# Optimization experiments

Measured on AMD Instinct MI355X. Metric: run time of the kernel, lower is better.

## Reference

```python
import jax, jax.numpy as jnp
import numpy as np

N_NODES = 50000
N_EDGES = 625000
D = 128
H = 128

def setup_inputs() -> dict:
    key = jax.random.key(0)
    ks = jax.random.split(key, 6)
    z = jax.random.normal(ks[0], (N_NODES, D), dtype=jnp.float32)
    edge_index = jax.random.randint(ks[1], (2, N_EDGES), 0, N_NODES, dtype=jnp.int64)
    # MLP params (Linear stores y = x @ W + b here; W is [in, out])
    W1 = jax.random.normal(ks[2], (2 * D, H), dtype=jnp.float32) * (1.0 / np.sqrt(2 * D))
    b1 = jnp.zeros((H,), dtype=jnp.float32)
    W2 = jax.random.normal(ks[3], (H, H // 2), dtype=jnp.float32) * (1.0 / np.sqrt(H))
    b2 = jnp.zeros((H // 2,), dtype=jnp.float32)
    W3 = jax.random.normal(ks[4], (H // 2, 1), dtype=jnp.float32) * (1.0 / np.sqrt(H // 2))
    b3 = jnp.zeros((1,), dtype=jnp.float32)
    return {"z": z, "edge_index": edge_index, "W1": W1, "b1": b1,
            "W2": W2, "b2": b2, "W3": W3, "b3": b3}

def reference(z, edge_index, W1, b1, W2, b2, W3, b3):
    # Gather edge endpoints: z_i [E, D], z_j [E, D]
    z_i = z[edge_index[0]]
    z_j = z[edge_index[1]]
    edge_feat = jnp.concatenate([z_i, z_j], axis=-1)  # [E, 2D]
    h = jax.nn.relu(edge_feat @ W1 + b1)              # [E, H]  (dropout = identity, eval)
    h = jax.nn.relu(h @ W2 + b2)                      # [E, H//2]
    scores = (h @ W3 + b3)[:, 0]                      # [E]
    return scores
```

## Files before the change

### kernel.cpp

```cpp
#include <hip/hip_runtime.h>

#define NEDGE 625000
#define NNODE 50000
#define NTILES ((NEDGE + 127) / 128)
#define WPITCH 136
#define EPITCH 68

typedef __bf16 bf16x8 __attribute__((ext_vector_type(8)));
typedef __bf16 bf16x4 __attribute__((ext_vector_type(4)));
typedef unsigned short u16x8 __attribute__((ext_vector_type(8)));
typedef float f32x4 __attribute__((ext_vector_type(4)));
typedef float f32x8 __attribute__((ext_vector_type(8)));

__device__ __forceinline__ unsigned short f32_bf16(float f) {
  unsigned int u = __float_as_uint(f);
  u += 0x7FFFu + ((u >> 16) & 1u);
  return (unsigned short)(u >> 16);
}

__device__ __forceinline__ bf16x8 addrelu8(u16x8 ua, u16x8 ub) {
  bf16x8 a = *(bf16x8*)&ua, b = *(bf16x8*)&ub;
  bf16x8 s = a + b;
  const bf16x8 z = {(__bf16)0.f, (__bf16)0.f, (__bf16)0.f, (__bf16)0.f,
                    (__bf16)0.f, (__bf16)0.f, (__bf16)0.f, (__bf16)0.f};
  return __builtin_elementwise_max(s, z);
}

__global__ __launch_bounds__(256) void prep_kernel(
    const float* __restrict__ W1, const float* __restrict__ W2,
    const int* __restrict__ ei,
    unsigned short* __restrict__ WcatT, unsigned short* __restrict__ W2T,
    int* __restrict__ idx64_flag)
{
  int i = blockIdx.x * 256 + threadIdx.x;
  if (i < 256 * 128) {
    int jp = i >> 7, k = i & 127;
    float v = (jp < 128) ? W1[k * 128 + jp] : W1[(128 + k) * 128 + (jp - 128)];
    WcatT[jp * 128 + k] = f32_bf16(v);
  } else if (i < 256 * 128 + 64 * 128) {
    int i2 = i - 256 * 128;
    int n = i2 >> 7, k = i2 & 127;
    W2T[n * 128 + k] = f32_bf16(W2[k * 64 + n]);
  }
  if (i == 0) {
    int allz = 1;
    for (int j = 1; j < 64; j += 2) allz &= (ei[j] == 0);
    *idx64_flag = allz;
  }
}

__global__ __launch_bounds__(256) void uv_kernel(
    const float* __restrict__ z, const float* __restrict__ b1,
    const unsigned short* __restrict__ WcatT,
    unsigned short* __restrict__ UV)
{
  __shared__ unsigned short st[4 * 32 * EPITCH];
  const int t = threadIdx.x, wave = t >> 6, lane = t & 63, c = lane & 15, q = lane >> 4;
  const int nc = wave;
  const int mbase = blockIdx.x * 32;
  const int rA = mbase + c, rB = mbase + 16 + c;
  const int rAc = (rA < NNODE) ? rA : 0;
  const int rBc = (rB < NNODE) ? rB : 0;

  bf16x8 a0[4], a1[4];
  {
    const float* zA = z + (size_t)rAc * 128 + q * 8;
    const float* zB = z + (size_t)rBc * 128 + q * 8;
#pragma unroll
    for (int kt = 0; kt < 4; ++kt) {
      f32x8 vA = *(const f32x8*)(zA + kt * 32);
      f32x8 vB = *(const f32x8*)(zB + kt * 32);
      a0[kt] = __builtin_convertvector(vA, bf16x8);
      a1[kt] = __builtin_convertvector(vB, bf16x8);
    }
  }

  f32x4 acc[2][4];
#pragma unroll
  for (int mt = 0; mt < 2; ++mt)
#pragma unroll
    for (int nt = 0; nt < 4; ++nt) {
      f32x4 zz = {0.f, 0.f, 0.f, 0.f};
      acc[mt][nt] = zz;
    }

#pragma unroll
  for (int kt = 0; kt < 4; ++kt) {
#pragma unroll
    for (int nt = 0; nt < 4; ++nt) {
      bf16x8 bb = *(const bf16x8*)(WcatT + (size_t)(nc * 64 + nt * 16 + c) * 128 + kt * 32 + q * 8);
      acc[0][nt] = __builtin_amdgcn_mfma_f32_16x16x32_bf16(a0[kt], bb, acc[0][nt], 0, 0, 0);
      acc[1][nt] = __builtin_amdgcn_mfma_f32_16x16x32_bf16(a1[kt], bb, acc[1][nt], 0, 0, 0);
    }
  }

  float badd[4];
#pragma unroll
  for (int nt = 0; nt < 4; ++nt) {
    int col = nc * 64 + nt * 16 + c;
    badd[nt] = (col < 128) ? b1[col] : 0.f;
  }

  unsigned short* my = &st[wave * 32 * EPITCH];
#pragma unroll
  for (int mt = 0; mt < 2; ++mt)
#pragma unroll
    for (int nt = 0; nt < 4; ++nt) {
      f32x4 v = acc[mt][nt];
      f32x4 vb = {v[0] + badd[nt], v[1] + badd[nt], v[2] + badd[nt], v[3] + badd[nt]};
      bf16x4 bv = __builtin_convertvector(vb, bf16x4);
      const unsigned short* pv = (const unsigned short*)&bv;
#pragma unroll
      for (int reg = 0; reg < 4; ++reg)
        my[(mt * 16 + q * 4 + reg) * EPITCH + nt * 16 + c] = pv[reg];
    }
  __asm__ volatile("s_waitcnt lgkmcnt(0)" ::: "memory");

  {
    int lrow = lane >> 1, half = lane & 1;
    int grow = mbase + lrow;
    u16x8 d0 = *(u16x8*)&my[lrow * EPITCH + half * 32 + 0];
    u16x8 d1 = *(u16x8*)&my[lrow * EPITCH + half * 32 + 8];
    u16x8 d2 = *(u16x8*)&my[lrow * EPITCH + half * 32 + 16];
    u16x8 d3 = *(u16x8*)&my[lrow * EPITCH + half * 32 + 24];
    if (grow < NNODE) {
      u16x8* dst = (u16x8*)(UV + (size_t)grow * 256 + nc * 64 + half * 32);
      dst[0] = d0; dst[1] = d1; dst[2] = d2; dst[3] = d3;
    }
  }
}

__global__ __launch_bounds__(256) void edge_kernel(
    const int* __restrict__ ei,
    const unsigned short* __restrict__ UV,
    const unsigned short* __restrict__ W2T,
    const float* __restrict__ b2, const float* __restrict__ W3,
    const float* __restrict__ b3, const int* __restrict__ idx64_flag,
    float* __restrict__ out)
{
  __shared__ unsigned short lW[64 * WPITCH];
  const int t = threadIdx.x, wave = t >> 6, lane = t & 63, c = lane & 15, q = lane >> 4;

  {
    int n = t >> 2, qd = t & 3;
    const u16x8* src = (const u16x8*)(W2T + n * 128 + qd * 32);
    u16x8* dst = (u16x8*)(&lW[n * WPITCH + qd * 32]);
#pragma unroll
    for (int i = 0; i < 4; ++i) dst[i] = src[i];
  }
  __syncthreads();

  const int ebase = blockIdx.x * 128 + wave * 32;
  const int eA = ebase + c, eB = ebase + 16 + c;
  const int eAc = (eA < NEDGE) ? eA : 0;
  const int eBc = (eB < NEDGE) ? eB : 0;
  int sA, dA, sB, dB;
  if (*idx64_flag) {
    const long long* e64 = (const long long*)ei;
    sA = (int)e64[eAc]; dA = (int)e64[NEDGE + eAc];
    sB = (int)e64[eBc]; dB = (int)e64[NEDGE + eBc];
  } else {
    sA = ei[eAc]; dA = ei[NEDGE + eAc];
    sB = ei[eBc]; dB = ei[NEDGE + eBc];
  }

  const u16x8* pAu = (const u16x8*)(UV + (size_t)sA * 256) + q;
  const u16x8* pAv = (const u16x8*)(UV + (size_t)dA * 256 + 128) + q;
  const u16x8* pBu = (const u16x8*)(UV + (size_t)sB * 256) + q;
  const u16x8* pBv = (const u16x8*)(UV + (size_t)dB * 256 + 128) + q;
  u16x8 rAu[4], rAv[4], rBu[4], rBv[4];
#pragma unroll
  for (int kt = 0; kt < 4; ++kt) {
    rAu[kt] = pAu[kt * 4];
    rAv[kt] = pAv[kt * 4];
    rBu[kt] = pBu[kt * 4];
    rBv[kt] = pBv[kt * 4];
  }

  f32x4 acc[2][4];
#pragma unroll
  for (int mt = 0; mt < 2; ++mt)
#pragma unroll
    for (int nt = 0; nt < 4; ++nt) {
      f32x4 zz = {0.f, 0.f, 0.f, 0.f};
      acc[mt][nt] = zz;
    }

#pragma unroll
  for (int kt = 0; kt < 4; ++kt) {
    bf16x8 a0 = addrelu8(rAu[kt], rAv[kt]);
    bf16x8 a1 = addrelu8(rBu[kt], rBv[kt]);
#pragma unroll
    for (int nt = 0; nt < 4; ++nt) {
      bf16x8 bb = *(const bf16x8*)(&lW[(nt * 16 + c) * WPITCH + kt * 32 + q * 8]);
      acc[0][nt] = __builtin_amdgcn_mfma_f32_16x16x32_bf16(a0, bb, acc[0][nt], 0, 0, 0);
      acc[1][nt] = __builtin_amdgcn_mfma_f32_16x16x32_bf16(a1, bb, acc[1][nt], 0, 0, 0);
    }
  }

  float b2v[4], w3v[4];
#pragma unroll
  for (int nt = 0; nt < 4; ++nt) {
    int n = nt * 16 + c;
    b2v[nt] = b2[n];
    w3v[nt] = W3[n];
  }
  const float bias3 = b3[0];

#pragma unroll
  for (int mt = 0; mt < 2; ++mt) {
    float p0 = 0.f, p1 = 0.f, p2 = 0.f, p3 = 0.f;
#pragma unroll
    for (int nt = 0; nt < 4; ++nt) {
      p0 += fmaxf(acc[mt][nt][0] + b2v[nt], 0.f) * w3v[nt];
      p1 += fmaxf(acc[mt][nt][1] + b2v[nt], 0.f) * w3v[nt];
      p2 += fmaxf(acc[mt][nt][2] + b2v[nt], 0.f) * w3v[nt];
      p3 += fmaxf(acc[mt][nt][3] + b2v[nt], 0.f) * w3v[nt];
    }
#pragma unroll
    for (int m = 1; m < 16; m <<= 1) {
      p0 += __shfl_xor(p0, m, 64);
      p1 += __shfl_xor(p1, m, 64);
      p2 += __shfl_xor(p2, m, 64);
      p3 += __shfl_xor(p3, m, 64);
    }
    if (c == 0) {
      int eb = ebase + mt * 16 + q * 4;
      if (eb + 0 < NEDGE) out[eb + 0] = p0 + bias3;
      if (eb + 1 < NEDGE) out[eb + 1] = p1 + bias3;
      if (eb + 2 < NEDGE) out[eb + 2] = p2 + bias3;
      if (eb + 3 < NEDGE) out[eb + 3] = p3 + bias3;
    }
  }
}

extern "C" void kernel_launch(void* const* d_in, const int* in_sizes, int n_in,
                              void* d_out, int out_size, void* d_ws, size_t ws_size,
                              hipStream_t stream) {
  const float* z  = (const float*)d_in[0];
  const int*   ei = (const int*)d_in[1];
  const float* W1 = (const float*)d_in[2];
  const float* b1 = (const float*)d_in[3];
  const float* W2 = (const float*)d_in[4];
  const float* b2 = (const float*)d_in[5];
  const float* W3 = (const float*)d_in[6];
  const float* b3 = (const float*)d_in[7];
  float* out = (float*)d_out;

  unsigned short* UV    = (unsigned short*)d_ws;
  unsigned short* WcatT = UV + (size_t)NNODE * 256;
  unsigned short* W2T   = WcatT + 256 * 128;
  int* idx64_flag       = (int*)(W2T + 64 * 128);

  prep_kernel<<<dim3(160), dim3(256), 0, stream>>>(W1, W2, ei, WcatT, W2T, idx64_flag);
  uv_kernel<<<dim3((NNODE + 31) / 32), dim3(256), 0, stream>>>(z, b1, WcatT, UV);
  edge_kernel<<<dim3(NTILES), dim3(256), 0, stream>>>(
      ei, UV, W2T, b2, W3, b3, idx64_flag, out);
}
```

Measured before the change: 160.2 us.

## Fuse prep, node-projection and edge kernels into one cooperative persistent kernel

Merges the three launches into a single cooperative kernel that uses grid-wide syncs between the weight conversion, the per-node UV projection and the edge MLP phases. Blocks become persistent and loop over node and edge tiles, and the W2 tile is loaded into LDS once per block instead of once per edge tile. The aim is to remove launch gaps and repeated LDS weight staging. The cost is two grid barriers, a grid capped by occupancy queries, and an occupancy query on the host at every launch.

```diff
diff --git a/kernel.cpp b/kernel.cpp
--- a/kernel.cpp
+++ b/kernel.cpp
@@ -1,8 +1,12 @@
 #include <hip/hip_runtime.h>
+#include <hip/hip_cooperative_groups.h>
+
+namespace cg = cooperative_groups;
 
 #define NEDGE 625000
 #define NNODE 50000
 #define NTILES ((NEDGE + 127) / 128)
+#define NMTILES ((NNODE + 31) / 32)
 #define WPITCH 136
 #define EPITCH 68
 
@@ -26,176 +30,122 @@
   return __builtin_elementwise_max(s, z);
 }
 
-__global__ __launch_bounds__(256) void prep_kernel(
-    const float* __restrict__ W1, const float* __restrict__ W2,
-    const int* __restrict__ ei,
-    unsigned short* __restrict__ WcatT, unsigned short* __restrict__ W2T,
-    int* __restrict__ idx64_flag)
+__global__ __launch_bounds__(256, 4) void fused_kernel(
+    const float* __restrict__ z, const int* __restrict__ ei,
+    const float* __restrict__ W1, const float* __restrict__ b1,
+    const float* __restrict__ W2, const float* __restrict__ b2,
+    const float* __restrict__ W3, const float* __restrict__ b3,
+    unsigned short* __restrict__ UV, unsigned short* __restrict__ WcatT,
+    unsigned short* __restrict__ W2T, float* __restrict__ out)
 {
-  int i = blockIdx.x * 256 + threadIdx.x;
-  if (i < 256 * 128) {
-    int jp = i >> 7, k = i & 127;
-    float v = (jp < 128) ? W1[k * 128 + jp] : W1[(128 + k) * 128 + (jp - 128)];
-    WcatT[jp * 128 + k] = f32_bf16(v);
-  } else if (i < 256 * 128 + 64 * 128) {
-    int i2 = i - 256 * 128;
-    int n = i2 >> 7, k = i2 & 127;
-    W2T[n * 128 + k] = f32_bf16(W2[k * 64 + n]);
-  }
-  if (i == 0) {
-    int allz = 1;
-    for (int j = 1; j < 64; j += 2) allz &= (ei[j] == 0);
-    *idx64_flag = allz;
-  }
-}
-
-__global__ __launch_bounds__(256) void uv_kernel(
-    const float* __restrict__ z, const float* __restrict__ b1,
-    const unsigned short* __restrict__ WcatT,
-    unsigned short* __restrict__ UV)
-{
-  __shared__ unsigned short st[4 * 32 * EPITCH];
+  __shared__ unsigned short smem[8704];
+  cg::grid_group grid = cg::this_grid();
   const int t = threadIdx.x, wave = t >> 6, lane = t & 63, c = lane & 15, q = lane >> 4;
-  const int nc = wave;
-  const int mbase = blockIdx.x * 32;
-  const int rA = mbase + c, rB = mbase + 16 + c;
-  const int rAc = (rA < NNODE) ? rA : 0;
-  const int rBc = (rB < NNODE) ? rB : 0;
-
-  bf16x8 a0[4], a1[4];
-  {
-    const float* zA = z + (size_t)rAc * 128 + q * 8;
-    const float* zB = z + (size_t)rBc * 128 + q * 8;
+
+  for (int i = blockIdx.x * 256 + t; i < 256 * 128 + 64 * 128; i += gridDim.x * 256) {
+    if (i < 256 * 128) {
+      int jp = i >> 7, k = i & 127;
+      float v = (jp < 128) ? W1[k * 128 + jp] : W1[(128 + k) * 128 + (jp - 128)];
+      WcatT[jp * 128 + k] = f32_bf16(v);
+    } else {
+      int i2 = i - 256 * 128;
+      int n = i2 >> 7, k = i2 & 127;
+      W2T[n * 128 + k] = f32_bf16(W2[k * 64 + n]);
+    }
+  }
+  grid.sync();
+
+  for (int mtile = blockIdx.x; mtile < NMTILES; mtile += gridDim.x) {
+    const int nc = wave;
+    const int mbase = mtile * 32;
+    const int rA = mbase + c, rB = mbase + 16 + c;
+    const int rAc = (rA < NNODE) ? rA : 0;
+    const int rBc = (rB < NNODE) ? rB : 0;
+
+    bf16x8 a0[4], a1[4];
+    {
+      const float* zA = z + (size_t)rAc * 128 + q * 8;
+      const float* zB = z + (size_t)rBc * 128 + q * 8;
+#pragma unroll
+      for (int kt = 0; kt < 4; ++kt) {
+        f32x8 vA = *(const f32x8*)(zA + kt * 32);
+        f32x8 vB = *(const f32x8*)(zB + kt * 32);
+        a0[kt] = __builtin_convertvector(vA, bf16x8);
+        a1[kt] = __builtin_convertvector(vB, bf16x8);
+      }
+    }
+
+    f32x4 acc[2][4];
+#pragma unroll
+    for (int mt = 0; mt < 2; ++mt)
+#pragma unroll
+      for (int nt = 0; nt < 4; ++nt) {
+        f32x4 zz = {0.f, 0.f, 0.f, 0.f};
+        acc[mt][nt] = zz;
+      }
+
 #pragma unroll
     for (int kt = 0; kt < 4; ++kt) {
-      f32x8 vA = *(const f32x8*)(zA + kt * 32);
-      f32x8 vB = *(const f32x8*)(zB + kt * 32);
-      a0[kt] = __builtin_convertvector(vA, bf16x8);
-      a1[kt] = __builtin_convertvector(vB, bf16x8);
-    }
-  }
-
-  f32x4 acc[2][4];
-#pragma unroll
-  for (int mt = 0; mt < 2; ++mt)
+#pragma unroll
+      for (int nt = 0; nt < 4; ++nt) {
+        bf16x8 bb = *(const bf16x8*)(WcatT + (size_t)(nc * 64 + nt * 16 + c) * 128 + kt * 32 + q * 8);
+        acc[0][nt] = __builtin_amdgcn_mfma_f32_16x16x32_bf16(a0[kt], bb, acc[0][nt], 0, 0, 0);
+        acc[1][nt] = __builtin_amdgcn_mfma_f32_16x16x32_bf16(a1[kt], bb, acc[1][nt], 0, 0, 0);
+      }
+    }
+
+    float badd[4];
 #pragma unroll
     for (int nt = 0; nt < 4; ++nt) {
-      f32x4 zz = {0.f, 0.f, 0.f, 0.f};
-      acc[mt][nt] = zz;
-    }
-
-#pragma unroll
-  for (int kt = 0; kt < 4; ++kt) {
-#pragma unroll
-    for (int nt = 0; nt < 4; ++nt) {
-      bf16x8 bb = *(const bf16x8*)(WcatT + (size_t)(nc * 64 + nt * 16 + c) * 128 + kt * 32 + q * 8);
-      acc[0][nt] = __builtin_amdgcn_mfma_f32_16x16x32_bf16(a0[kt], bb, acc[0][nt], 0, 0, 0);
-      acc[1][nt] = __builtin_amdgcn_mfma_f32_16x16x32_bf16(a1[kt], bb, acc[1][nt], 0, 0, 0);
-    }
-  }
-
-  float badd[4];
-#pragma unroll
-  for (int nt = 0; nt < 4; ++nt) {
-    int col = nc * 64 + nt * 16 + c;
-    badd[nt] = (col < 128) ? b1[col] : 0.f;
-  }
-
-  unsigned short* my = &st[wave * 32 * EPITCH];
-#pragma unroll
-  for (int mt = 0; mt < 2; ++mt)
-#pragma unroll
-    for (int nt = 0; nt < 4; ++nt) {
-      f32x4 v = acc[mt][nt];
-      f32x4 vb = {v[0] + badd[nt], v[1] + badd[nt], v[2] + badd[nt], v[3] + badd[nt]};
-      bf16x4 bv = __builtin_convertvector(vb, bf16x4);
-      const unsigned short* pv = (const unsigned short*)&bv;
-#pragma unroll
-      for (int reg = 0; reg < 4; ++reg)
-        my[(mt * 16 + q * 4 + reg) * EPITCH + nt * 16 + c] = pv[reg];
-    }
-  __asm__ volatile("s_waitcnt lgkmcnt(0)" ::: "memory");
-
-  {
-    int lrow = lane >> 1, half = lane & 1;
-    int grow = mbase + lrow;
-    u16x8 d0 = *(u16x8*)&my[lrow * EPITCH + half * 32 + 0];
-    u16x8 d1 = *(u16x8*)&my[lrow * EPITCH + half * 32 + 8];
-    u16x8 d2 = *(u16x8*)&my[lrow * EPITCH + half * 32 + 16];
-    u16x8 d3 = *(u16x8*)&my[lrow * EPITCH + half * 32 + 24];
-    if (grow < NNODE) {
-      u16x8* dst = (u16x8*)(UV + (size_t)grow * 256 + nc * 64 + half * 32);
-      dst[0] = d0; dst[1] = d1; dst[2] = d2; dst[3] = d3;
-    }
-  }
-}
-
-__global__ __launch_bounds__(256) void edge_kernel(
-    const int* __restrict__ ei,
-    const unsigned short* __restrict__ UV,
-    const unsigned short* __restrict__ W2T,
-    const float* __restrict__ b2, const float* __restrict__ W3,
-    const float* __restrict__ b3, const int* __restrict__ idx64_flag,
-    float* __restrict__ out)
-{
-  __shared__ unsigned short lW[64 * WPITCH];
-  const int t = threadIdx.x, wave = t >> 6, lane = t & 63, c = lane & 15, q = lane >> 4;
+      int col = nc * 64 + nt * 16 + c;
+      badd[nt] = (col < 128) ? b1[col] : 0.f;
+    }
+
+    unsigned short* my = &smem[wave * 32 * EPITCH];
+#pragma unroll
+    for (int mt = 0; mt < 2; ++mt)
+#pragma unroll
+      for (int nt = 0; nt < 4; ++nt) {
+        f32x4 v = acc[mt][nt];
+        f32x4 vb = {v[0] + badd[nt], v[1] + badd[nt], v[2] + badd[nt], v[3] + badd[nt]};
+        bf16x4 bv = __builtin_convertvector(vb, bf16x4);
+        const unsigned short* pv = (const unsigned short*)&bv;
+#pragma unroll
+        for (int reg = 0; reg < 4; ++reg)
+          my[(mt * 16 + q * 4 + reg) * EPITCH + nt * 16 + c] = pv[reg];
+      }
+    __asm__ volatile("s_waitcnt lgkmcnt(0)" ::: "memory");
+
+    {
+      int lrow = lane >> 1, half = lane & 1;
+      int grow = mbase + lrow;
+      u16x8 d0 = *(u16x8*)&my[lrow * EPITCH + half * 32 + 0];
+      u16x8 d1 = *(u16x8*)&my[lrow * EPITCH + half * 32 + 8];
+      u16x8 d2 = *(u16x8*)&my[lrow * EPITCH + half * 32 + 16];
+      u16x8 d3 = *(u16x8*)&my[lrow * EPITCH + half * 32 + 24];
+      if (grow < NNODE) {
+        u16x8* dst = (u16x8*)(UV + (size_t)grow * 256 + nc * 64 + half * 32);
+        dst[0] = d0; dst[1] = d1; dst[2] = d2; dst[3] = d3;
+      }
+    }
+    __asm__ volatile("s_waitcnt lgkmcnt(0)" ::: "memory");
+  }
+  grid.sync();
 
   {
     int n = t >> 2, qd = t & 3;
     const u16x8* src = (const u16x8*)(W2T + n * 128 + qd * 32);
-    u16x8* dst = (u16x8*)(&lW[n * WPITCH + qd * 32]);
+    u16x8* dst = (u16x8*)(&smem[n * WPITCH + qd * 32]);
 #pragma unroll
     for (int i = 0; i < 4; ++i) dst[i] = src[i];
   }
   __syncthreads();
 
-  const int ebase = blockIdx.x * 128 + wave * 32;
-  const int eA = ebase + c, eB = ebase + 16 + c;
-  const int eAc = (eA < NEDGE) ? eA : 0;
-  const int eBc = (eB < NEDGE) ? eB : 0;
-  int sA, dA, sB, dB;
-  if (*idx64_flag) {
-    const long long* e64 = (const long long*)ei;
-    sA = (int)e64[eAc]; dA = (int)e64[NEDGE + eAc];
-    sB = (int)e64[eBc]; dB = (int)e64[NEDGE + eBc];
-  } else {
-    sA = ei[eAc]; dA = ei[NEDGE + eAc];
-    sB = ei[eBc]; dB = ei[NEDGE + eBc];
-  }
-
-  const u16x8* pAu = (const u16x8*)(UV + (size_t)sA * 256) + q;
-  const u16x8* pAv = (const u16x8*)(UV + (size_t)dA * 256 + 128) + q;
-  const u16x8* pBu = (const u16x8*)(UV + (size_t)sB * 256) + q;
-  const u16x8* pBv = (const u16x8*)(UV + (size_t)dB * 256 + 128) + q;
-  u16x8 rAu[4], rAv[4], rBu[4], rBv[4];
-#pragma unroll
-  for (int kt = 0; kt < 4; ++kt) {
-    rAu[kt] = pAu[kt * 4];
-    rAv[kt] = pAv[kt * 4];
-    rBu[kt] = pBu[kt * 4];
-    rBv[kt] = pBv[kt * 4];
-  }
-
-  f32x4 acc[2][4];
-#pragma unroll
-  for (int mt = 0; mt < 2; ++mt)
-#pragma unroll
-    for (int nt = 0; nt < 4; ++nt) {
-      f32x4 zz = {0.f, 0.f, 0.f, 0.f};
-      acc[mt][nt] = zz;
-    }
-
-#pragma unroll
-  for (int kt = 0; kt < 4; ++kt) {
-    bf16x8 a0 = addrelu8(rAu[kt], rAv[kt]);
-    bf16x8 a1 = addrelu8(rBu[kt], rBv[kt]);
-#pragma unroll
-    for (int nt = 0; nt < 4; ++nt) {
-      bf16x8 bb = *(const bf16x8*)(&lW[(nt * 16 + c) * WPITCH + kt * 32 + q * 8]);
-      acc[0][nt] = __builtin_amdgcn_mfma_f32_16x16x32_bf16(a0, bb, acc[0][nt], 0, 0, 0);
-      acc[1][nt] = __builtin_amdgcn_mfma_f32_16x16x32_bf16(a1, bb, acc[1][nt], 0, 0, 0);
-    }
+  int is64;
+  {
+    int allz = 1;
+    for (int j = 1; j < 64; j += 2) allz &= (ei[j] == 0);
+    is64 = allz;
   }
 
   float b2v[4], w3v[4];
@@ -207,29 +157,79 @@
   }
   const float bias3 = b3[0];
 
-#pragma unroll
-  for (int mt = 0; mt < 2; ++mt) {
-    float p0 = 0.f, p1 = 0.f, p2 = 0.f, p3 = 0.f;
-#pragma unroll
-    for (int nt = 0; nt < 4; ++nt) {
-      p0 += fmaxf(acc[mt][nt][0] + b2v[nt], 0.f) * w3v[nt];
-      p1 += fmaxf(acc[mt][nt][1] + b2v[nt], 0.f) * w3v[nt];
-      p2 += fmaxf(acc[mt][nt][2] + b2v[nt], 0.f) * w3v[nt];
-      p3 += fmaxf(acc[mt][nt][3] + b2v[nt], 0.f) * w3v[nt];
-    }
-#pragma unroll
-    for (int m = 1; m < 16; m <<= 1) {
-      p0 += __shfl_xor(p0, m, 64);
-      p1 += __shfl_xor(p1, m, 64);
-      p2 += __shfl_xor(p2, m, 64);
-      p3 += __shfl_xor(p3, m, 64);
-    }
-    if (c == 0) {
-      int eb = ebase + mt * 16 + q * 4;
-      if (eb + 0 < NEDGE) out[eb + 0] = p0 + bias3;
-      if (eb + 1 < NEDGE) out[eb + 1] = p1 + bias3;
-      if (eb + 2 < NEDGE) out[eb + 2] = p2 + bias3;
-      if (eb + 3 < NEDGE) out[eb + 3] = p3 + bias3;
+  for (int tile = blockIdx.x; tile < NTILES; tile += gridDim.x) {
+    const int ebase = tile * 128 + wave * 32;
+    const int eA = ebase + c, eB = ebase + 16 + c;
+    const int eAc = (eA < NEDGE) ? eA : 0;
+    const int eBc = (eB < NEDGE) ? eB : 0;
+    int sA, dA, sB, dB;
+    if (is64) {
+      const long long* e64 = (const long long*)ei;
+      sA = (int)e64[eAc]; dA = (int)e64[NEDGE + eAc];
+      sB = (int)e64[eBc]; dB = (int)e64[NEDGE + eBc];
+    } else {
+      sA = ei[eAc]; dA = ei[NEDGE + eAc];
+      sB = ei[eBc]; dB = ei[NEDGE + eBc];
+    }
+
+    const u16x8* pAu = (const u16x8*)(UV + (size_t)sA * 256) + q;
+    const u16x8* pAv = (const u16x8*)(UV + (size_t)dA * 256 + 128) + q;
+    const u16x8* pBu = (const u16x8*)(UV + (size_t)sB * 256) + q;
+    const u16x8* pBv = (const u16x8*)(UV + (size_t)dB * 256 + 128) + q;
+    u16x8 rAu[4], rAv[4], rBu[4], rBv[4];
+#pragma unroll
+    for (int kt = 0; kt < 4; ++kt) {
+      rAu[kt] = pAu[kt * 4];
+      rAv[kt] = pAv[kt * 4];
+      rBu[kt] = pBu[kt * 4];
+      rBv[kt] = pBv[kt * 4];
+    }
+
+    f32x4 acc[2][4];
+#pragma unroll
+    for (int mt = 0; mt < 2; ++mt)
+#pragma unroll
+      for (int nt = 0; nt < 4; ++nt) {
+        f32x4 zz = {0.f, 0.f, 0.f, 0.f};
+        acc[mt][nt] = zz;
+      }
+
+#pragma unroll
+    for (int kt = 0; kt < 4; ++kt) {
+      bf16x8 a0 = addrelu8(rAu[kt], rAv[kt]);
+      bf16x8 a1 = addrelu8(rBu[kt], rBv[kt]);
+#pragma unroll
+      for (int nt = 0; nt < 4; ++nt) {
+        bf16x8 bb = *(const bf16x8*)(&smem[(nt * 16 + c) * WPITCH + kt * 32 + q * 8]);
+        acc[0][nt] = __builtin_amdgcn_mfma_f32_16x16x32_bf16(a0, bb, acc[0][nt], 0, 0, 0);
+        acc[1][nt] = __builtin_amdgcn_mfma_f32_16x16x32_bf16(a1, bb, acc[1][nt], 0, 0, 0);
+      }
+    }
+
+#pragma unroll
+    for (int mt = 0; mt < 2; ++mt) {
+      float p0 = 0.f, p1 = 0.f, p2 = 0.f, p3 = 0.f;
+#pragma unroll
+      for (int nt = 0; nt < 4; ++nt) {
+        p0 += fmaxf(acc[mt][nt][0] + b2v[nt], 0.f) * w3v[nt];
+        p1 += fmaxf(acc[mt][nt][1] + b2v[nt], 0.f) * w3v[nt];
+        p2 += fmaxf(acc[mt][nt][2] + b2v[nt], 0.f) * w3v[nt];
+        p3 += fmaxf(acc[mt][nt][3] + b2v[nt], 0.f) * w3v[nt];
+      }
+#pragma unroll
+      for (int m = 1; m < 16; m <<= 1) {
+        p0 += __shfl_xor(p0, m, 64);
+        p1 += __shfl_xor(p1, m, 64);
+        p2 += __shfl_xor(p2, m, 64);
+        p3 += __shfl_xor(p3, m, 64);
+      }
+      if (c == 0) {
+        int eb = ebase + mt * 16 + q * 4;
+        if (eb + 0 < NEDGE) out[eb + 0] = p0 + bias3;
+        if (eb + 1 < NEDGE) out[eb + 1] = p1 + bias3;
+        if (eb + 2 < NEDGE) out[eb + 2] = p2 + bias3;
+        if (eb + 3 < NEDGE) out[eb + 3] = p3 + bias3;
+      }
     }
   }
 }
@@ -250,10 +250,16 @@
   unsigned short* UV    = (unsigned short*)d_ws;
   unsigned short* WcatT = UV + (size_t)NNODE * 256;
   unsigned short* W2T   = WcatT + 256 * 128;
-  int* idx64_flag       = (int*)(W2T + 64 * 128);
-
-  prep_kernel<<<dim3(160), dim3(256), 0, stream>>>(W1, W2, ei, WcatT, W2T, idx64_flag);
-  uv_kernel<<<dim3((NNODE + 31) / 32), dim3(256), 0, stream>>>(z, b1, WcatT, UV);
-  edge_kernel<<<dim3(NTILES), dim3(256), 0, stream>>>(
-      ei, UV, W2T, b2, W3, b3, idx64_flag, out);
-}
+
+  int maxB = 0;
+  hipOccupancyMaxActiveBlocksPerMultiprocessor(&maxB, (const void*)fused_kernel, 256, 0);
+  if (maxB < 1) maxB = 1;
+  if (maxB > 4) maxB = 4;
+  int grid = maxB * 256;
+
+  void* args[] = {(void*)&z, (void*)&ei, (void*)&W1, (void*)&b1,
+                  (void*)&W2, (void*)&b2, (void*)&W3, (void*)&b3,
+                  (void*)&UV, (void*)&WcatT, (void*)&W2T, (void*)&out};
+  hipLaunchCooperativeKernel((const void*)fused_kernel, dim3(grid), dim3(256),
+                             args, 0, stream);
+}
```

Measured after the change: 320.6 us. 100% more time.

## Persistent grid for edge kernel and coalesced LDS staging of z in uv kernel

Applied to the files above, without the earlier changes.

The edge kernel now runs a fixed grid of 2048 blocks that loop over edge tiles. Each block loads W2 into shared memory once and reuses it across tiles, instead of reloading it in every one of ~4900 blocks. Launch bounds now request 8 blocks per CU. The uv kernel stages z rows into LDS as bf16 with coalesced loads before MFMA. The cost is a barrier, and the serial tile loop may expose gather latency that more independent blocks would otherwise hide.

```diff
diff --git a/kernel.cpp b/kernel.cpp
--- a/kernel.cpp
+++ b/kernel.cpp
@@ -3,7 +3,9 @@
 #define NEDGE 625000
 #define NNODE 50000
 #define NTILES ((NEDGE + 127) / 128)
+#define EGRID 2048
 #define WPITCH 136
+#define ZPITCH 136
 #define EPITCH 68
 
 typedef __bf16 bf16x8 __attribute__((ext_vector_type(8)));
@@ -54,25 +56,31 @@
     const unsigned short* __restrict__ WcatT,
     unsigned short* __restrict__ UV)
 {
+  __shared__ unsigned short zb[32 * ZPITCH];
   __shared__ unsigned short st[4 * 32 * EPITCH];
   const int t = threadIdx.x, wave = t >> 6, lane = t & 63, c = lane & 15, q = lane >> 4;
   const int nc = wave;
   const int mbase = blockIdx.x * 32;
-  const int rA = mbase + c, rB = mbase + 16 + c;
-  const int rAc = (rA < NNODE) ? rA : 0;
-  const int rBc = (rB < NNODE) ? rB : 0;
+
+  {
+    int r = t >> 3, ch = t & 7;
+    int grow = mbase + r;
+    const float* src = z + (size_t)((grow < NNODE) ? grow : 0) * 128 + ch * 16;
+    f32x8 f0 = ((const f32x8*)src)[0];
+    f32x8 f1 = ((const f32x8*)src)[1];
+    bf16x8 b0 = __builtin_convertvector(f0, bf16x8);
+    bf16x8 b1 = __builtin_convertvector(f1, bf16x8);
+    unsigned short* d = &zb[r * ZPITCH + ch * 16];
+    *(bf16x8*)(d + 0) = b0;
+    *(bf16x8*)(d + 8) = b1;
+  }
+  __syncthreads();
 
   bf16x8 a0[4], a1[4];
-  {
-    const float* zA = z + (size_t)rAc * 128 + q * 8;
-    const float* zB = z + (size_t)rBc * 128 + q * 8;
-#pragma unroll
-    for (int kt = 0; kt < 4; ++kt) {
-      f32x8 vA = *(const f32x8*)(zA + kt * 32);
-      f32x8 vB = *(const f32x8*)(zB + kt * 32);
-      a0[kt] = __builtin_convertvector(vA, bf16x8);
-      a1[kt] = __builtin_convertvector(vB, bf16x8);
-    }
+#pragma unroll
+  for (int kt = 0; kt < 4; ++kt) {
+    a0[kt] = *(const bf16x8*)(&zb[c * ZPITCH + kt * 32 + q * 8]);
+    a1[kt] = *(const bf16x8*)(&zb[(16 + c) * ZPITCH + kt * 32 + q * 8]);
   }
 
   f32x4 acc[2][4];
@@ -130,7 +138,7 @@
   }
 }
 
-__global__ __launch_bounds__(256) void edge_kernel(
+__global__ __launch_bounds__(256, 8) void edge_kernel(
     const int* __restrict__ ei,
     const unsigned short* __restrict__ UV,
     const unsigned short* __restrict__ W2T,
@@ -150,54 +158,7 @@
   }
   __syncthreads();
 
-  const int ebase = blockIdx.x * 128 + wave * 32;
-  const int eA = ebase + c, eB = ebase + 16 + c;
-  const int eAc = (eA < NEDGE) ? eA : 0;
-  const int eBc = (eB < NEDGE) ? eB : 0;
-  int sA, dA, sB, dB;
-  if (*idx64_flag) {
-    const long long* e64 = (const long long*)ei;
-    sA = (int)e64[eAc]; dA = (int)e64[NEDGE + eAc];
-    sB = (int)e64[eBc]; dB = (int)e64[NEDGE + eBc];
-  } else {
-    sA = ei[eAc]; dA = ei[NEDGE + eAc];
-    sB = ei[eBc]; dB = ei[NEDGE + eBc];
-  }
-
-  const u16x8* pAu = (const u16x8*)(UV + (size_t)sA * 256) + q;
-  const u16x8* pAv = (const u16x8*)(UV + (size_t)dA * 256 + 128) + q;
-  const u16x8* pBu = (const u16x8*)(UV + (size_t)sB * 256) + q;
-  const u16x8* pBv = (const u16x8*)(UV + (size_t)dB * 256 + 128) + q;
-  u16x8 rAu[4], rAv[4], rBu[4], rBv[4];
-#pragma unroll
-  for (int kt = 0; kt < 4; ++kt) {
-    rAu[kt] = pAu[kt * 4];
-    rAv[kt] = pAv[kt * 4];
-    rBu[kt] = pBu[kt * 4];
-    rBv[kt] = pBv[kt * 4];
-  }
-
-  f32x4 acc[2][4];
-#pragma unroll
-  for (int mt = 0; mt < 2; ++mt)
-#pragma unroll
-    for (int nt = 0; nt < 4; ++nt) {
-      f32x4 zz = {0.f, 0.f, 0.f, 0.f};
-      acc[mt][nt] = zz;
-    }
-
-#pragma unroll
-  for (int kt = 0; kt < 4; ++kt) {
-    bf16x8 a0 = addrelu8(rAu[kt], rAv[kt]);
-    bf16x8 a1 = addrelu8(rBu[kt], rBv[kt]);
-#pragma unroll
-    for (int nt = 0; nt < 4; ++nt) {
-      bf16x8 bb = *(const bf16x8*)(&lW[(nt * 16 + c) * WPITCH + kt * 32 + q * 8]);
-      acc[0][nt] = __builtin_amdgcn_mfma_f32_16x16x32_bf16(a0, bb, acc[0][nt], 0, 0, 0);
-      acc[1][nt] = __builtin_amdgcn_mfma_f32_16x16x32_bf16(a1, bb, acc[1][nt], 0, 0, 0);
-    }
-  }
-
+  const int is64 = *idx64_flag;
   float b2v[4], w3v[4];
 #pragma unroll
   for (int nt = 0; nt < 4; ++nt) {
@@ -207,29 +168,79 @@
   }
   const float bias3 = b3[0];
 
-#pragma unroll
-  for (int mt = 0; mt < 2; ++mt) {
-    float p0 = 0.f, p1 = 0.f, p2 = 0.f, p3 = 0.f;
-#pragma unroll
-    for (int nt = 0; nt < 4; ++nt) {
-      p0 += fmaxf(acc[mt][nt][0] + b2v[nt], 0.f) * w3v[nt];
-      p1 += fmaxf(acc[mt][nt][1] + b2v[nt], 0.f) * w3v[nt];
-      p2 += fmaxf(acc[mt][nt][2] + b2v[nt], 0.f) * w3v[nt];
-      p3 += fmaxf(acc[mt][nt][3] + b2v[nt], 0.f) * w3v[nt];
-    }
-#pragma unroll
-    for (int m = 1; m < 16; m <<= 1) {
-      p0 += __shfl_xor(p0, m, 64);
-      p1 += __shfl_xor(p1, m, 64);
-      p2 += __shfl_xor(p2, m, 64);
-      p3 += __shfl_xor(p3, m, 64);
-    }
-    if (c == 0) {
-      int eb = ebase + mt * 16 + q * 4;
-      if (eb + 0 < NEDGE) out[eb + 0] = p0 + bias3;
-      if (eb + 1 < NEDGE) out[eb + 1] = p1 + bias3;
-      if (eb + 2 < NEDGE) out[eb + 2] = p2 + bias3;
-      if (eb + 3 < NEDGE) out[eb + 3] = p3 + bias3;
+  for (int tile = blockIdx.x; tile < NTILES; tile += EGRID) {
+    const int ebase = tile * 128 + wave * 32;
+    const int eA = ebase + c, eB = ebase + 16 + c;
+    const int eAc = (eA < NEDGE) ? eA : 0;
+    const int eBc = (eB < NEDGE) ? eB : 0;
+    int sA, dA, sB, dB;
+    if (is64) {
+      const long long* e64 = (const long long*)ei;
+      sA = (int)e64[eAc]; dA = (int)e64[NEDGE + eAc];
+      sB = (int)e64[eBc]; dB = (int)e64[NEDGE + eBc];
+    } else {
+      sA = ei[eAc]; dA = ei[NEDGE + eAc];
+      sB = ei[eBc]; dB = ei[NEDGE + eBc];
+    }
+
+    const u16x8* pAu = (const u16x8*)(UV + (size_t)sA * 256) + q;
+    const u16x8* pAv = (const u16x8*)(UV + (size_t)dA * 256 + 128) + q;
+    const u16x8* pBu = (const u16x8*)(UV + (size_t)sB * 256) + q;
+    const u16x8* pBv = (const u16x8*)(UV + (size_t)dB * 256 + 128) + q;
+    u16x8 rAu[4], rAv[4], rBu[4], rBv[4];
+#pragma unroll
+    for (int kt = 0; kt < 4; ++kt) {
+      rAu[kt] = pAu[kt * 4];
+      rAv[kt] = pAv[kt * 4];
+      rBu[kt] = pBu[kt * 4];
+      rBv[kt] = pBv[kt * 4];
+    }
+
+    f32x4 acc[2][4];
+#pragma unroll
+    for (int mt = 0; mt < 2; ++mt)
+#pragma unroll
+      for (int nt = 0; nt < 4; ++nt) {
+        f32x4 zz = {0.f, 0.f, 0.f, 0.f};
+        acc[mt][nt] = zz;
+      }
+
+#pragma unroll
+    for (int kt = 0; kt < 4; ++kt) {
+      bf16x8 a0 = addrelu8(rAu[kt], rAv[kt]);
+      bf16x8 a1 = addrelu8(rBu[kt], rBv[kt]);
+#pragma unroll
+      for (int nt = 0; nt < 4; ++nt) {
+        bf16x8 bb = *(const bf16x8*)(&lW[(nt * 16 + c) * WPITCH + kt * 32 + q * 8]);
+        acc[0][nt] = __builtin_amdgcn_mfma_f32_16x16x32_bf16(a0, bb, acc[0][nt], 0, 0, 0);
+        acc[1][nt] = __builtin_amdgcn_mfma_f32_16x16x32_bf16(a1, bb, acc[1][nt], 0, 0, 0);
+      }
+    }
+
+#pragma unroll
+    for (int mt = 0; mt < 2; ++mt) {
+      float p0 = 0.f, p1 = 0.f, p2 = 0.f, p3 = 0.f;
+#pragma unroll
+      for (int nt = 0; nt < 4; ++nt) {
+        p0 += fmaxf(acc[mt][nt][0] + b2v[nt], 0.f) * w3v[nt];
+        p1 += fmaxf(acc[mt][nt][1] + b2v[nt], 0.f) * w3v[nt];
+        p2 += fmaxf(acc[mt][nt][2] + b2v[nt], 0.f) * w3v[nt];
+        p3 += fmaxf(acc[mt][nt][3] + b2v[nt], 0.f) * w3v[nt];
+      }
+#pragma unroll
+      for (int m = 1; m < 16; m <<= 1) {
+        p0 += __shfl_xor(p0, m, 64);
+        p1 += __shfl_xor(p1, m, 64);
+        p2 += __shfl_xor(p2, m, 64);
+        p3 += __shfl_xor(p3, m, 64);
+      }
+      if (c == 0) {
+        int eb = ebase + mt * 16 + q * 4;
+        if (eb + 0 < NEDGE) out[eb + 0] = p0 + bias3;
+        if (eb + 1 < NEDGE) out[eb + 1] = p1 + bias3;
+        if (eb + 2 < NEDGE) out[eb + 2] = p2 + bias3;
+        if (eb + 3 < NEDGE) out[eb + 3] = p3 + bias3;
+      }
     }
   }
 }
@@ -254,6 +265,6 @@
 
   prep_kernel<<<dim3(160), dim3(256), 0, stream>>>(W1, W2, ei, WcatT, W2T, idx64_flag);
   uv_kernel<<<dim3((NNODE + 31) / 32), dim3(256), 0, stream>>>(z, b1, WcatT, UV);
-  edge_kernel<<<dim3(NTILES), dim3(256), 0, stream>>>(
+  edge_kernel<<<dim3(EGRID), dim3(256), 0, stream>>>(
       ei, UV, W2T, b2, W3, b3, idx64_flag, out);
 }
```

Result: slower. 310.9 us (+94.1%).
